# Performance work log

Measured on AMD Instinct MI355X. Metric: run time of the kernel, lower is better.

## Reference

```python
import jax, jax.numpy as jnp
import numpy as np

MAX_ITER = 3  # module default init kwarg
B, S = 16, 128


def setup_inputs() -> dict:
    key = jax.random.key(0)
    k1, k2, k3 = jax.random.split(key, 3)
    s_span = jax.random.normal(k1, (B, S, S), dtype=jnp.float32)
    s_pair = jax.random.normal(k2, (B, S, S, S), dtype=jnp.float32)
    mask = jax.random.randint(k3, (B, S, S), 0, 2).astype(jnp.bool_)
    return {"s_span": s_span, "s_pair": s_pair, "mask": mask}


def reference(s_span, s_pair, mask):
    # Faithful batch-first translation of MFVIConstituency.mfvi + sigmoid.
    # torch code works in [S, S, B] layout; here we keep [B, S, S].
    seq_len = mask.shape[1]
    idx = jnp.arange(seq_len)
    # ls[i,j]=min(i,j), rs[i,j]=max(i,j) (stack(where(ones)).sort(0) trick)
    ls = jnp.minimum(idx[:, None], idx[None, :])  # [S, S]
    rs = jnp.maximum(idx[:, None], idx[None, :])  # [S, S]
    # exclude k == min(i,j) and k == max(i,j): [S, S, S] over (i, j, k)
    ne = (ls[:, :, None] != idx[None, None, :]) & (rs[:, :, None] != idx[None, None, :])
    # span_mask broadcast in torch aligns trailing dims -> indexed at (j, k):
    # mask2o[b,i,j,k] &= mask[b,k,j] | mask[b,j,k]
    span = mask | jnp.swapaxes(mask, 1, 2)  # [B, S, S] symmetric
    # mask2o[b,i,j,k] = mask[b,i,j] & ne[i,j,k] & span[b,j,k]
    mask2o = mask[:, :, :, None] & ne[None, :, :, :] & span[:, None, :, :]
    sp = s_pair * mask2o.astype(s_pair.dtype)  # [B, S, S, S]
    q = s_span
    for _ in range(MAX_ITER):
        q = jax.nn.sigmoid(q)
        # q_new[b,i,j] = s_span[b,i,j] + sum_k q[b,i,k] * sp[b,i,j,k]
        q = s_span + jnp.einsum('bik,bijk->bij', q, sp)
    return jax.nn.sigmoid(q)  # marginals [B, S, S]
```

## Files before the change

### kernel.cpp

```cpp
#include <hip/hip_runtime.h>
#include <hip/hip_bf16.h>


#define S 128
#define MB_STRIDE 132
#define PART_STRIDE 33

__global__ __launch_bounds__(256, 2) void pack_masks(
    const int* __restrict__ mask, unsigned* __restrict__ spanw,
    unsigned* __restrict__ miw)
{
    __shared__ unsigned char mb[S * MB_STRIDE];
    const int t = threadIdx.x, b = blockIdx.x;
    const int* mrow = mask + (long long)b * (S * S);
    #pragma unroll
    for (int s2 = 0; s2 < 16; ++s2) {
        int f4 = t + 256 * s2;
        int j  = f4 >> 5;
        int k0 = (f4 & 31) * 4;
        int4 v = *(const int4*)(mrow + f4 * 4);
        unsigned packed = (v.x ? 1u : 0u)
                        | ((v.y ? 1u : 0u) << 8)
                        | ((v.z ? 1u : 0u) << 16)
                        | ((v.w ? 1u : 0u) << 24);
        *(unsigned*)(mb + j * MB_STRIDE + k0) = packed;
    }
    __syncthreads();
    #pragma unroll
    for (int r = 0; r < 2; ++r) {
        int task = t * 2 + r;
        int j = task >> 2, w = task & 3;
        unsigned sbits = 0, mbits = 0;
        #pragma unroll
        for (int c = 0; c < 32; ++c) {
            int k = w * 32 + c;
            unsigned mjk = mb[j * MB_STRIDE + k];
            unsigned mkj = mb[k * MB_STRIDE + j];
            sbits |= ((mjk | mkj) ? 1u : 0u) << c;
            mbits |= (mjk ? 1u : 0u) << c;
        }
        spanw[(b * S + j) * 4 + w] = sbits;
        miw  [(b * S + j) * 4 + w] = mbits;
    }
}

__global__ __launch_bounds__(256, 4) void mfvi_main(
    const float* __restrict__ s_span,
    const float* __restrict__ s_pair,
    const unsigned* __restrict__ spanw,
    const unsigned* __restrict__ miw,
    float* __restrict__ out)
{
    __shared__ float    part[S * PART_STRIDE];
    __shared__ unsigned sw_l[S * 4];
    __shared__ float    prow[S];
    __shared__ unsigned miw_l[4];

    const int t  = threadIdx.x;
    const int bi = blockIdx.x;
    const int i  = bi & (S - 1);
    const int b  = bi >> 7;
    const int row0 = t >> 5;
    const int k0   = (t & 31) * 4;
    const float* tile = s_pair + (long long)bi * (S * S);

    float4 v[16];
    #pragma unroll
    for (int s = 0; s < 16; ++s)
        v[s] = *(const float4*)(tile + (row0 + 8 * s) * S + k0);

    if (t < S)  *(uint4*)&sw_l[t * 4] = *(const uint4*)&spanw[(b * S + t) * 4];
    if (t < 4)  miw_l[t] = miw[(b * S + i) * 4 + t];
    float sv = 0.f;
    if (t < S) {
        sv = s_span[(long long)bi * S + t];
        prow[t] = 1.0f / (1.0f + __expf(-sv));
    }
    __syncthreads();

    #pragma unroll
    for (int s = 0; s < 16; ++s) {
        int j = row0 + 8 * s;
        unsigned sw = sw_l[j * 4 + (k0 >> 5)];
        bool mi = (miw_l[j >> 5] >> (j & 31)) & 1u;
        int lo = min(i, j), hi = max(i, j);
        int bb = k0 & 31;
        if (!(mi && ((sw >> (bb + 0)) & 1u) && (k0 + 0) != lo && (k0 + 0) != hi)) v[s].x = 0.f;
        if (!(mi && ((sw >> (bb + 1)) & 1u) && (k0 + 1) != lo && (k0 + 1) != hi)) v[s].y = 0.f;
        if (!(mi && ((sw >> (bb + 2)) & 1u) && (k0 + 2) != lo && (k0 + 2) != hi)) v[s].z = 0.f;
        if (!(mi && ((sw >> (bb + 3)) & 1u) && (k0 + 3) != lo && (k0 + 3) != hi)) v[s].w = 0.f;
    }

    const int pcol = t & 31;
    for (int it = 0; it < 3; ++it) {
        float4 p = *(const float4*)&prow[k0];
        #pragma unroll
        for (int s = 0; s < 16; ++s) {
            int j = row0 + 8 * s;
            float acc = v[s].x * p.x + v[s].y * p.y + v[s].z * p.z + v[s].w * p.w;
            part[j * PART_STRIDE + pcol] = acc;
        }
        __syncthreads();
        if (t < S) {
            float sum = 0.f;
            #pragma unroll
            for (int c = 0; c < 32; ++c) sum += part[t * PART_STRIDE + c];
            float q = sv + sum;
            if (it < 2) prow[t] = 1.0f / (1.0f + __expf(-q));
            else        out[(long long)bi * S + t] = 1.0f / (1.0f + __expf(-q));
        }
        if (it < 2) __syncthreads();
    }
}

extern "C" void kernel_launch(void* const* d_in, const int* in_sizes, int n_in,
                              void* d_out, int out_size, void* d_ws, size_t ws_size,
                              hipStream_t stream) {
    const float* s_span = (const float*)d_in[0];
    const float* s_pair = (const float*)d_in[1];
    const int*   mask   = (const int*)d_in[2];
    float*       out    = (float*)d_out;

    int num_rows = in_sizes[0] / S;
    int B        = in_sizes[2] / (S * S);

    unsigned* ws_span = (unsigned*)d_ws;
    unsigned* ws_mi   = ws_span + (size_t)B * S * 4;

    pack_masks<<<B, 256, 0, stream>>>(mask, ws_span, ws_mi);
    mfvi_main<<<num_rows, 256, 0, stream>>>(s_span, s_pair, ws_span, ws_mi, out);
}
```

Before: 208.3 us.

## Compact active mask rows and skip loading masked-out s_pair rows

Builds a compacted list of active j indices for row i via ballot/popcount, loads only those s_pair rows, and writes sigmoid(s_span) directly for inactive rows, whose pair contribution is zero. This cuts global memory traffic roughly in proportion to the mask density. It also replaces the division in the sigmoid with a hardware reciprocal, turns the masking into bitwise ANDs, and fully unrolls the iteration loop. The compaction adds an extra barrier and some divergence.

```diff
diff --git a/kernel.cpp b/kernel.cpp
--- a/kernel.cpp
+++ b/kernel.cpp
@@ -5,6 +5,10 @@
 #define S 128
 #define MB_STRIDE 132
 #define PART_STRIDE 33
+
+static __device__ __forceinline__ float fsig(float x) {
+    return __builtin_amdgcn_rcpf(1.0f + __expf(-x));
+}
 
 __global__ __launch_bounds__(256, 2) void pack_masks(
     const int* __restrict__ mask, unsigned* __restrict__ spanw,
@@ -51,63 +55,104 @@
     const unsigned* __restrict__ miw,
     float* __restrict__ out)
 {
-    __shared__ float    part[S * PART_STRIDE];
-    __shared__ unsigned sw_l[S * 4];
-    __shared__ float    prow[S];
-    __shared__ unsigned miw_l[4];
+    __shared__ float         part[S * PART_STRIDE];
+    __shared__ unsigned      sw_l[S * 4];
+    __shared__ float         prow[S];
+    __shared__ float         qsv [S];
+    __shared__ unsigned char act [S];
+    __shared__ int           nact_s;
 
     const int t  = threadIdx.x;
     const int bi = blockIdx.x;
     const int i  = bi & (S - 1);
     const int b  = bi >> 7;
     const int row0 = t >> 5;
-    const int k0   = (t & 31) * 4;
+    const int c4   = (t & 31) * 4;
     const float* tile = s_pair + (long long)bi * (S * S);
+
+    if (t < S) *(uint4*)&sw_l[t * 4] = *(const uint4*)&spanw[(b * S + t) * 4];
+    if (t < S) {
+        float sv = s_span[(long long)bi * S + t];
+        qsv[t]  = sv;
+        prow[t] = fsig(sv);
+    }
+    if (t < 64) {
+        unsigned w0 = miw[(b * S + i) * 4 + (t >> 5)];
+        bool a0 = (w0 >> (t & 31)) & 1u;
+        unsigned long long b0 = __ballot(a0);
+        int p0 = __popcll(b0 & ((1ull << t) - 1ull));
+        if (a0) act[p0] = (unsigned char)t;
+        int n0 = __popcll(b0);
+        int j1 = t + 64;
+        unsigned w1 = miw[(b * S + i) * 4 + (j1 >> 5)];
+        bool a1 = (w1 >> (j1 & 31)) & 1u;
+        unsigned long long b1 = __ballot(a1);
+        int p1 = n0 + __popcll(b1 & ((1ull << t) - 1ull));
+        if (a1) act[p1] = (unsigned char)j1;
+        if (t == 0) nact_s = n0 + __popcll(b1);
+    }
+    __syncthreads();
+    const int nact = nact_s;
+
+    if (t < S) {
+        bool mine = (miw[(b * S + i) * 4 + (t >> 5)] >> (t & 31)) & 1u;
+        if (!mine) out[(long long)bi * S + t] = prow[t];
+    }
 
     float4 v[16];
     #pragma unroll
-    for (int s = 0; s < 16; ++s)
-        v[s] = *(const float4*)(tile + (row0 + 8 * s) * S + k0);
-
-    if (t < S)  *(uint4*)&sw_l[t * 4] = *(const uint4*)&spanw[(b * S + t) * 4];
-    if (t < 4)  miw_l[t] = miw[(b * S + i) * 4 + t];
-    float sv = 0.f;
-    if (t < S) {
-        sv = s_span[(long long)bi * S + t];
-        prow[t] = 1.0f / (1.0f + __expf(-sv));
+    for (int s = 0; s < 16; ++s) {
+        int idx = row0 + 8 * s;
+        if (idx < nact) {
+            int j = act[idx];
+            v[s] = *(const float4*)(tile + j * S + c4);
+        } else {
+            v[s] = make_float4(0.f, 0.f, 0.f, 0.f);
+        }
     }
-    __syncthreads();
 
     #pragma unroll
     for (int s = 0; s < 16; ++s) {
-        int j = row0 + 8 * s;
-        unsigned sw = sw_l[j * 4 + (k0 >> 5)];
-        bool mi = (miw_l[j >> 5] >> (j & 31)) & 1u;
-        int lo = min(i, j), hi = max(i, j);
-        int bb = k0 & 31;
-        if (!(mi && ((sw >> (bb + 0)) & 1u) && (k0 + 0) != lo && (k0 + 0) != hi)) v[s].x = 0.f;
-        if (!(mi && ((sw >> (bb + 1)) & 1u) && (k0 + 1) != lo && (k0 + 1) != hi)) v[s].y = 0.f;
-        if (!(mi && ((sw >> (bb + 2)) & 1u) && (k0 + 2) != lo && (k0 + 2) != hi)) v[s].z = 0.f;
-        if (!(mi && ((sw >> (bb + 3)) & 1u) && (k0 + 3) != lo && (k0 + 3) != hi)) v[s].w = 0.f;
+        int idx = row0 + 8 * s;
+        if (idx < nact) {
+            int j = act[idx];
+            unsigned cw = sw_l[j * 4 + (c4 >> 5)];
+            int lo = i < j ? i : j, hi = i < j ? j : i;
+            if ((lo >> 5) == (c4 >> 5)) cw &= ~(1u << (lo & 31));
+            if ((hi >> 5) == (c4 >> 5)) cw &= ~(1u << (hi & 31));
+            unsigned cs = cw >> (c4 & 31);
+            int m0 = ((int)(cs << 31)) >> 31;
+            int m1 = ((int)(cs << 30)) >> 31;
+            int m2 = ((int)(cs << 29)) >> 31;
+            int m3 = ((int)(cs << 28)) >> 31;
+            v[s].x = __int_as_float(__float_as_int(v[s].x) & m0);
+            v[s].y = __int_as_float(__float_as_int(v[s].y) & m1);
+            v[s].z = __int_as_float(__float_as_int(v[s].z) & m2);
+            v[s].w = __int_as_float(__float_as_int(v[s].w) & m3);
+        }
     }
 
     const int pcol = t & 31;
+    #pragma unroll
     for (int it = 0; it < 3; ++it) {
-        float4 p = *(const float4*)&prow[k0];
+        float4 p = *(const float4*)&prow[c4];
         #pragma unroll
         for (int s = 0; s < 16; ++s) {
-            int j = row0 + 8 * s;
-            float acc = v[s].x * p.x + v[s].y * p.y + v[s].z * p.z + v[s].w * p.w;
-            part[j * PART_STRIDE + pcol] = acc;
+            int idx = row0 + 8 * s;
+            if (idx < nact) {
+                float acc = v[s].x * p.x + v[s].y * p.y + v[s].z * p.z + v[s].w * p.w;
+                part[idx * PART_STRIDE + pcol] = acc;
+            }
         }
         __syncthreads();
-        if (t < S) {
+        if (t < nact) {
+            int j = act[t];
             float sum = 0.f;
             #pragma unroll
             for (int c = 0; c < 32; ++c) sum += part[t * PART_STRIDE + c];
-            float q = sv + sum;
-            if (it < 2) prow[t] = 1.0f / (1.0f + __expf(-q));
-            else        out[(long long)bi * S + t] = 1.0f / (1.0f + __expf(-q));
+            float q = qsv[j] + sum;
+            if (it < 2) prow[j] = fsig(q);
+            else        out[(long long)bi * S + j] = fsig(q);
         }
         if (it < 2) __syncthreads();
     }
```

Measured after the change: 191.2 us. 1.09x faster.
